# Performance work log

Hardware: AMD Instinct MI355X
Metric: run time of the kernel (lower is better)

## Reference

```python
import jax, jax.numpy as jnp
import numpy as np

B, N_E, E_DIM = 131072, 1024, 64
BETA = 0.25


def setup_inputs() -> dict:
    key = jax.random.key(0)
    kz, kw = jax.random.split(key)
    z = jax.random.normal(kz, (B, E_DIM), dtype=jnp.float32)
    # nn.Embedding init: uniform(-1/n_e, 1/n_e)
    emb_w = jax.random.uniform(kw, (N_E, E_DIM), dtype=jnp.float32,
                               minval=-1.0 / N_E, maxval=1.0 / N_E)
    return {"z": z, "emb_w": emb_w}


def reference(z, emb_w):
    beta = jnp.float32(BETA)
    # pairwise squared distances: [B, n_e]
    d = (jnp.sum(z * z, axis=1, keepdims=True)
         + jnp.sum(emb_w * emb_w, axis=1)
         - 2.0 * jnp.einsum('bd,nd->bn', z, emb_w))
    idx = jnp.argmin(d, axis=1)                      # [B]
    z_q = jnp.take(emb_w, idx, axis=0)               # [B, e_dim]
    # legacy=False branch
    loss = (beta * jnp.mean((jax.lax.stop_gradient(z_q) - z) ** 2)
            + jnp.mean((z_q - jax.lax.stop_gradient(z)) ** 2))
    # straight-through estimator
    z_q_st = z + jax.lax.stop_gradient(z_q - z)
    # torch.var is unbiased (ddof=1)
    v = jnp.var(idx.astype(jnp.float32), ddof=1)
    return (z_q_st, loss, idx, v)
```

## Files before the change

### kernel.cpp

```cpp
#include <hip/hip_runtime.h>
#include <stdint.h>


typedef __attribute__((ext_vector_type(8))) __bf16 bf16x8;
typedef __attribute__((ext_vector_type(4))) float f32x4;

#define OUT_LOSS 8388608
#define OUT_IDX  8388609
#define OUT_VAR  8519681

#define WS_LOSS  0
#define WS_S1    4096
#define WS_S2    8192
#define WS_EFRAG 12288
#define WS_EE    143360

__device__ __forceinline__ void gld_lds16(const void* g, void* l) {
  __builtin_amdgcn_global_load_lds(
      (const __attribute__((address_space(1))) unsigned*)g,
      (__attribute__((address_space(3))) unsigned*)l, 16, 0, 0);
}

__global__ void vq_prep(const float* __restrict__ emb, char* __restrict__ ws) {
  bf16x8* efrag = (bf16x8*)(ws + WS_EFRAG);
  float* eeoff = (float*)(ws + WS_EE);
  const int t = blockIdx.x;
  const int l = threadIdx.x;
  const int n = t * 16 + (l & 15);
  const int kb0 = (l >> 4) * 8;
  const float* er = emb + n * 64;
  for (int j = 0; j < 2; ++j) {
    const int kb = j * 32 + kb0;
    bf16x8 h;
#pragma unroll
    for (int i = 0; i < 8; ++i) h[i] = (__bf16)(-2.0f * er[kb + i]);
    efrag[(t * 2 + j) * 64 + l] = h;
  }
  if (l < 16) {
    const float* e2 = emb + (t * 16 + l) * 64;
    float s = 0.f;
#pragma unroll
    for (int d = 0; d < 64; ++d) s += e2[d] * e2[d];
    eeoff[t * 16 + l] = s + 0.5f;
  }
}

__global__ void __launch_bounds__(256) vq_main(
    const float* __restrict__ z, const float* __restrict__ emb,
    float* __restrict__ out, char* __restrict__ ws) {
  __shared__ char smfrag[2][16384];
  __shared__ float see[1024];
  __shared__ float sL[4];
  __shared__ int sA[4], sB[4];

  const int tid = threadIdx.x;
  const int wave = tid >> 6, lane = tid & 63;
  const int lr = lane & 15, ksl = lane >> 4;
  const int k0 = ksl * 8;
  const int row_base = blockIdx.x * 128 + wave * 32;

#define STAGE(ph, buf)                                                         \
  {                                                                            \
    _Pragma("unroll")                                                          \
    for (int i_ = 0; i_ < 4; ++i_)                                             \
      gld_lds16(ws + WS_EFRAG + (ph) * 16384 + i_ * 4096 + wave * 1024 + lane * 16, \
                smfrag[buf] + i_ * 4096 + wave * 1024);                        \
  }

  gld_lds16(ws + WS_EE + wave * 1024 + lane * 16, (char*)see + wave * 1024);
  STAGE(0, 0);
  STAGE(1, 1);

  bf16x8 zfa0, zfa1, zfb0, zfb1;
  float zza, zzb;
  {
    const float* zra = z + (size_t)(row_base + lr) * 64;
    const float* zrb = z + (size_t)(row_base + 16 + lr) * 64;
    f32x4 a0 = *(const f32x4*)(zra + k0);
    f32x4 a1 = *(const f32x4*)(zra + k0 + 4);
    f32x4 a2 = *(const f32x4*)(zra + 32 + k0);
    f32x4 a3 = *(const f32x4*)(zra + 32 + k0 + 4);
    f32x4 b0 = *(const f32x4*)(zrb + k0);
    f32x4 b1 = *(const f32x4*)(zrb + k0 + 4);
    f32x4 b2 = *(const f32x4*)(zrb + 32 + k0);
    f32x4 b3 = *(const f32x4*)(zrb + 32 + k0 + 4);
    float sa = 0.f, sb = 0.f;
#pragma unroll
    for (int i = 0; i < 4; ++i) {
      zfa0[i] = (__bf16)a0[i]; zfa0[4 + i] = (__bf16)a1[i];
      zfa1[i] = (__bf16)a2[i]; zfa1[4 + i] = (__bf16)a3[i];
      zfb0[i] = (__bf16)b0[i]; zfb0[4 + i] = (__bf16)b1[i];
      zfb1[i] = (__bf16)b2[i]; zfb1[4 + i] = (__bf16)b3[i];
      sa += a0[i] * a0[i] + a1[i] * a1[i] + a2[i] * a2[i] + a3[i] * a3[i];
      sb += b0[i] * b0[i] + b1[i] * b1[i] + b2[i] * b2[i] + b3[i] * b3[i];
    }
    sa += __shfl_xor(sa, 16, 64); sa += __shfl_xor(sa, 32, 64);
    sb += __shfl_xor(sb, 16, 64); sb += __shfl_xor(sb, 32, 64);
    zza = sa; zzb = sb;
  }

  unsigned rka = 0xFFFFFFFFu, rkb = 0xFFFFFFFFu;
  const unsigned k4 = (unsigned)(ksl * 4);

#pragma unroll
  for (int ph = 0; ph < 8; ++ph) {
    if (ph < 7) { asm volatile("s_waitcnt vmcnt(4)" ::: "memory"); }
    else       { asm volatile("s_waitcnt vmcnt(0)" ::: "memory"); }
    __builtin_amdgcn_sched_barrier(0);
    __builtin_amdgcn_s_barrier();
    const bf16x8* sfrag = (const bf16x8*)(smfrag[ph & 1]);
#pragma unroll
    for (int tt = 0; tt < 8; ++tt) {
      const int g = ph * 8 + tt;
      bf16x8 e0 = sfrag[(tt * 2 + 0) * 64 + lane];
      bf16x8 e1 = sfrag[(tt * 2 + 1) * 64 + lane];
      const f32x4 ee = *(const f32x4*)(see + g * 16 + ksl * 4);
      f32x4 a = __builtin_amdgcn_mfma_f32_16x16x32_bf16(e0, zfa0, ee, 0, 0, 0);
      a = __builtin_amdgcn_mfma_f32_16x16x32_bf16(e1, zfa1, a, 0, 0, 0);
      f32x4 b = __builtin_amdgcn_mfma_f32_16x16x32_bf16(e0, zfb0, ee, 0, 0, 0);
      b = __builtin_amdgcn_mfma_f32_16x16x32_bf16(e1, zfb1, b, 0, 0, 0);
      const unsigned tw = (unsigned)(g * 16);
      {
        const unsigned t0 = (__float_as_uint(a[0]) & 0xFFFFFC00u) | (k4 + 0);
        const unsigned t1 = (__float_as_uint(a[1]) & 0xFFFFFC00u) | (k4 + 1);
        const unsigned t2 = (__float_as_uint(a[2]) & 0xFFFFFC00u) | (k4 + 2);
        const unsigned t3 = (__float_as_uint(a[3]) & 0xFFFFFC00u) | (k4 + 3);
        rka = min(rka, min(min(t0, t1), min(t2, t3)) | tw);
      }
      {
        const unsigned t0 = (__float_as_uint(b[0]) & 0xFFFFFC00u) | (k4 + 0);
        const unsigned t1 = (__float_as_uint(b[1]) & 0xFFFFFC00u) | (k4 + 1);
        const unsigned t2 = (__float_as_uint(b[2]) & 0xFFFFFC00u) | (k4 + 2);
        const unsigned t3 = (__float_as_uint(b[3]) & 0xFFFFFC00u) | (k4 + 3);
        rkb = min(rkb, min(min(t0, t1), min(t2, t3)) | tw);
      }
    }
    __builtin_amdgcn_s_barrier();
    if (ph < 6) STAGE(ph + 2, ph & 1);
  }
#undef STAGE

  rka = min(rka, (unsigned)__shfl_xor((int)rka, 16, 64));
  rka = min(rka, (unsigned)__shfl_xor((int)rka, 32, 64));
  rkb = min(rkb, (unsigned)__shfl_xor((int)rkb, 16, 64));
  rkb = min(rkb, (unsigned)__shfl_xor((int)rkb, 32, 64));

  const int erow = lane >> 1, eseg = lane & 1;
  const int src = erow & 15;
  const unsigned ka = (unsigned)__shfl((int)rka, src, 64);
  const unsigned kb = (unsigned)__shfl((int)rkb, src, 64);
  const float za = __shfl(zza, src, 64);
  const float zb = __shfl(zzb, src, 64);
  const unsigned k = (erow < 16) ? ka : kb;
  const float zzv = (erow < 16) ? za : zb;
  const unsigned idx = k & 1023u;
  const size_t rowg = (size_t)row_base + erow;
  const f32x4* ep = (const f32x4*)(emb + (size_t)idx * 64 + eseg * 32);
  f32x4* op = (f32x4*)(out + rowg * 64 + eseg * 32);
#pragma unroll
  for (int c = 0; c < 8; ++c) op[c] = ep[c];

  float ls = 0.f; int s1 = 0, s2 = 0;
  if (eseg == 0) {
    ls = zzv + __uint_as_float(k & 0xFFFFFC00u) - 0.5f;
    s1 = (int)idx;
    s2 = (int)(idx * idx);
    out[OUT_IDX + rowg] = (float)idx;
  }
#pragma unroll
  for (int off = 1; off < 64; off <<= 1) {
    ls += __shfl_xor(ls, off, 64);
    s1 += __shfl_xor(s1, off, 64);
    s2 += __shfl_xor(s2, off, 64);
  }
  if (lane == 0) { sL[wave] = ls; sA[wave] = s1; sB[wave] = s2; }
  __syncthreads();
  if (tid == 0) {
    float L = 0; int a = 0, b = 0;
#pragma unroll
    for (int w = 0; w < 4; ++w) { L += sL[w]; a += sA[w]; b += sB[w]; }
    ((float*)(ws + WS_LOSS))[blockIdx.x] = L;
    ((int*)(ws + WS_S1))[blockIdx.x] = a;
    ((int*)(ws + WS_S2))[blockIdx.x] = b;
  }
}

__global__ void vq_final(float* __restrict__ out, const char* __restrict__ ws) {
  const int t = threadIdx.x;
  const float* lp = (const float*)(ws + WS_LOSS);
  const int* p1 = (const int*)(ws + WS_S1);
  const int* p2 = (const int*)(ws + WS_S2);
  double L = 0; long long a = 0, b = 0;
#pragma unroll
  for (int kk = 0; kk < 4; ++kk) {
    const int i = t + 256 * kk;
    L += (double)lp[i];
    a += (long long)p1[i];
    b += (long long)p2[i];
  }
#pragma unroll
  for (int off = 1; off < 64; off <<= 1) {
    L += __shfl_xor(L, off, 64);
    a += __shfl_xor(a, off, 64);
    b += __shfl_xor(b, off, 64);
  }
  __shared__ double sL[4];
  __shared__ long long sA[4], sB[4];
  const int wave = t >> 6, lane = t & 63;
  if (lane == 0) { sL[wave] = L; sA[wave] = a; sB[wave] = b; }
  __syncthreads();
  if (t == 0) {
    double Lt = 0; long long at = 0, bt = 0;
#pragma unroll
    for (int w = 0; w < 4; ++w) { Lt += sL[w]; at += sA[w]; bt += sB[w]; }
    out[OUT_LOSS] = (float)(1.25 * Lt / 8388608.0);
    long long num = bt * 131072LL - at * at;
    out[OUT_VAR] = (float)((double)num / (131072.0 * 131071.0));
  }
}

extern "C" void kernel_launch(void* const* d_in, const int* in_sizes, int n_in,
                              void* d_out, int out_size, void* d_ws, size_t ws_size,
                              hipStream_t stream) {
  (void)in_sizes; (void)n_in; (void)out_size; (void)ws_size;
  const float* z = (const float*)d_in[0];
  const float* emb = (const float*)d_in[1];
  float* out = (float*)d_out;
  char* ws = (char*)d_ws;
  vq_prep<<<64, 64, 0, stream>>>(emb, ws);
  vq_main<<<1024, 256, 0, stream>>>(z, emb, out, ws);
  vq_final<<<1, 256, 0, stream>>>(out, ws);
}
```

Measured before the change: 45.70 us.

## Use 512-thread blocks with triple-buffered LDS codebook staging and denser argmin keys

Blocks grow to 8 waves handling 256 rows each, so every codebook fragment staged into LDS is reused by twice as many rows. The LDS ring goes from two buffers to three, which lets the next prefetch be issued right after the barrier and removes the second barrier per phase. MFMA sections get raised wave priority, and the z loads are issued before the staging loads. The argmin key changes from masking the low mantissa bits to shifting the float left by 10, with a 0.875 bias so distances stay within a fixed exponent range, which keeps more mantissa precision in the key. The risk is lower occupancy and a distance-range assumption tied to the bias.

```diff
diff --git a/kernel.cpp b/kernel.cpp
--- a/kernel.cpp
+++ b/kernel.cpp
@@ -41,49 +41,51 @@
     float s = 0.f;
 #pragma unroll
     for (int d = 0; d < 64; ++d) s += e2[d] * e2[d];
-    eeoff[t * 16 + l] = s + 0.5f;
-  }
-}
-
-__global__ void __launch_bounds__(256) vq_main(
+    eeoff[t * 16 + l] = s + 0.875f;
+  }
+}
+
+__global__ void __launch_bounds__(512) vq_main(
     const float* __restrict__ z, const float* __restrict__ emb,
     float* __restrict__ out, char* __restrict__ ws) {
-  __shared__ char smfrag[2][16384];
+  __shared__ char smfrag[3][16384];
   __shared__ float see[1024];
-  __shared__ float sL[4];
-  __shared__ int sA[4], sB[4];
+  __shared__ float sL[8];
+  __shared__ int sA[8], sB[8];
 
   const int tid = threadIdx.x;
   const int wave = tid >> 6, lane = tid & 63;
   const int lr = lane & 15, ksl = lane >> 4;
   const int k0 = ksl * 8;
-  const int row_base = blockIdx.x * 128 + wave * 32;
-
-#define STAGE(ph, buf)                                                         \
-  {                                                                            \
-    _Pragma("unroll")                                                          \
-    for (int i_ = 0; i_ < 4; ++i_)                                             \
-      gld_lds16(ws + WS_EFRAG + (ph) * 16384 + i_ * 4096 + wave * 1024 + lane * 16, \
-                smfrag[buf] + i_ * 4096 + wave * 1024);                        \
-  }
-
-  gld_lds16(ws + WS_EE + wave * 1024 + lane * 16, (char*)see + wave * 1024);
+  const int row_base = blockIdx.x * 256 + wave * 32;
+
+#define STAGE(ph, buf)                                                          \
+  {                                                                             \
+    _Pragma("unroll")                                                           \
+    for (int i_ = 0; i_ < 2; ++i_)                                              \
+      gld_lds16(ws + WS_EFRAG + (ph) * 16384 + wave * 2048 + i_ * 1024 + lane * 16, \
+                smfrag[buf] + wave * 2048 + i_ * 1024);                         \
+  }
+
+  const float* zra = z + (size_t)(row_base + lr) * 64;
+  const float* zrb = z + (size_t)(row_base + 16 + lr) * 64;
+  f32x4 a0 = *(const f32x4*)(zra + k0);
+  f32x4 a1 = *(const f32x4*)(zra + k0 + 4);
+  f32x4 a2 = *(const f32x4*)(zra + 32 + k0);
+  f32x4 a3 = *(const f32x4*)(zra + 32 + k0 + 4);
+  f32x4 b0 = *(const f32x4*)(zrb + k0);
+  f32x4 b1 = *(const f32x4*)(zrb + k0 + 4);
+  f32x4 b2 = *(const f32x4*)(zrb + 32 + k0);
+  f32x4 b3 = *(const f32x4*)(zrb + 32 + k0 + 4);
+
+  if (wave < 4)
+    gld_lds16(ws + WS_EE + wave * 1024 + lane * 16, (char*)see + wave * 1024);
   STAGE(0, 0);
   STAGE(1, 1);
 
   bf16x8 zfa0, zfa1, zfb0, zfb1;
   float zza, zzb;
   {
-    const float* zra = z + (size_t)(row_base + lr) * 64;
-    const float* zrb = z + (size_t)(row_base + 16 + lr) * 64;
-    f32x4 a0 = *(const f32x4*)(zra + k0);
-    f32x4 a1 = *(const f32x4*)(zra + k0 + 4);
-    f32x4 a2 = *(const f32x4*)(zra + 32 + k0);
-    f32x4 a3 = *(const f32x4*)(zra + 32 + k0 + 4);
-    f32x4 b0 = *(const f32x4*)(zrb + k0);
-    f32x4 b1 = *(const f32x4*)(zrb + k0 + 4);
-    f32x4 b2 = *(const f32x4*)(zrb + 32 + k0);
-    f32x4 b3 = *(const f32x4*)(zrb + 32 + k0 + 4);
     float sa = 0.f, sb = 0.f;
 #pragma unroll
     for (int i = 0; i < 4; ++i) {
@@ -100,15 +102,16 @@
   }
 
   unsigned rka = 0xFFFFFFFFu, rkb = 0xFFFFFFFFu;
-  const unsigned k4 = (unsigned)(ksl * 4);
-
-#pragma unroll
+  const unsigned kj0 = (unsigned)(ksl * 4), kj1 = kj0 + 1, kj2 = kj0 + 2, kj3 = kj0 + 3;
+
   for (int ph = 0; ph < 8; ++ph) {
-    if (ph < 7) { asm volatile("s_waitcnt vmcnt(4)" ::: "memory"); }
-    else       { asm volatile("s_waitcnt vmcnt(0)" ::: "memory"); }
+    if (ph < 7) { asm volatile("s_waitcnt vmcnt(2)" ::: "memory"); }
+    else        { asm volatile("s_waitcnt vmcnt(0)" ::: "memory"); }
     __builtin_amdgcn_sched_barrier(0);
     __builtin_amdgcn_s_barrier();
-    const bf16x8* sfrag = (const bf16x8*)(smfrag[ph & 1]);
+    if (ph < 6) STAGE(ph + 2, (ph + 2) % 3);
+    const bf16x8* sfrag = (const bf16x8*)(smfrag[ph % 3]);
+    __builtin_amdgcn_s_setprio(1);
 #pragma unroll
     for (int tt = 0; tt < 8; ++tt) {
       const int g = ph * 8 + tt;
@@ -119,24 +122,23 @@
       a = __builtin_amdgcn_mfma_f32_16x16x32_bf16(e1, zfa1, a, 0, 0, 0);
       f32x4 b = __builtin_amdgcn_mfma_f32_16x16x32_bf16(e0, zfb0, ee, 0, 0, 0);
       b = __builtin_amdgcn_mfma_f32_16x16x32_bf16(e1, zfb1, b, 0, 0, 0);
-      const unsigned tw = (unsigned)(g * 16);
+      const unsigned g16 = (unsigned)(g * 16);
       {
-        const unsigned t0 = (__float_as_uint(a[0]) & 0xFFFFFC00u) | (k4 + 0);
-        const unsigned t1 = (__float_as_uint(a[1]) & 0xFFFFFC00u) | (k4 + 1);
-        const unsigned t2 = (__float_as_uint(a[2]) & 0xFFFFFC00u) | (k4 + 2);
-        const unsigned t3 = (__float_as_uint(a[3]) & 0xFFFFFC00u) | (k4 + 3);
-        rka = min(rka, min(min(t0, t1), min(t2, t3)) | tw);
+        const unsigned q0 = (__float_as_uint(a[0]) << 10) + kj0;
+        const unsigned q1 = (__float_as_uint(a[1]) << 10) + kj1;
+        const unsigned q2 = (__float_as_uint(a[2]) << 10) + kj2;
+        const unsigned q3 = (__float_as_uint(a[3]) << 10) + kj3;
+        rka = min(rka, min(min(q0, q1), min(q2, q3)) + g16);
       }
       {
-        const unsigned t0 = (__float_as_uint(b[0]) & 0xFFFFFC00u) | (k4 + 0);
-        const unsigned t1 = (__float_as_uint(b[1]) & 0xFFFFFC00u) | (k4 + 1);
-        const unsigned t2 = (__float_as_uint(b[2]) & 0xFFFFFC00u) | (k4 + 2);
-        const unsigned t3 = (__float_as_uint(b[3]) & 0xFFFFFC00u) | (k4 + 3);
-        rkb = min(rkb, min(min(t0, t1), min(t2, t3)) | tw);
+        const unsigned q0 = (__float_as_uint(b[0]) << 10) + kj0;
+        const unsigned q1 = (__float_as_uint(b[1]) << 10) + kj1;
+        const unsigned q2 = (__float_as_uint(b[2]) << 10) + kj2;
+        const unsigned q3 = (__float_as_uint(b[3]) << 10) + kj3;
+        rkb = min(rkb, min(min(q0, q1), min(q2, q3)) + g16);
       }
     }
-    __builtin_amdgcn_s_barrier();
-    if (ph < 6) STAGE(ph + 2, ph & 1);
+    __builtin_amdgcn_s_setprio(0);
   }
 #undef STAGE
 
@@ -162,7 +164,7 @@
 
   float ls = 0.f; int s1 = 0, s2 = 0;
   if (eseg == 0) {
-    ls = zzv + __uint_as_float(k & 0xFFFFFC00u) - 0.5f;
+    ls = zzv + __uint_as_float(0x3F400000u | (k >> 10)) - 0.875f;
     s1 = (int)idx;
     s2 = (int)(idx * idx);
     out[OUT_IDX + rowg] = (float)idx;
@@ -178,7 +180,7 @@
   if (tid == 0) {
     float L = 0; int a = 0, b = 0;
 #pragma unroll
-    for (int w = 0; w < 4; ++w) { L += sL[w]; a += sA[w]; b += sB[w]; }
+    for (int w = 0; w < 8; ++w) { L += sL[w]; a += sA[w]; b += sB[w]; }
     ((float*)(ws + WS_LOSS))[blockIdx.x] = L;
     ((int*)(ws + WS_S1))[blockIdx.x] = a;
     ((int*)(ws + WS_S2))[blockIdx.x] = b;
@@ -192,7 +194,7 @@
   const int* p2 = (const int*)(ws + WS_S2);
   double L = 0; long long a = 0, b = 0;
 #pragma unroll
-  for (int kk = 0; kk < 4; ++kk) {
+  for (int kk = 0; kk < 2; ++kk) {
     const int i = t + 256 * kk;
     L += (double)lp[i];
     a += (long long)p1[i];
@@ -204,15 +206,15 @@
     a += __shfl_xor(a, off, 64);
     b += __shfl_xor(b, off, 64);
   }
-  __shared__ double sL[4];
-  __shared__ long long sA[4], sB[4];
+  __shared__ double sLf[4];
+  __shared__ long long sAf[4], sBf[4];
   const int wave = t >> 6, lane = t & 63;
-  if (lane == 0) { sL[wave] = L; sA[wave] = a; sB[wave] = b; }
+  if (lane == 0) { sLf[wave] = L; sAf[wave] = a; sBf[wave] = b; }
   __syncthreads();
   if (t == 0) {
     double Lt = 0; long long at = 0, bt = 0;
 #pragma unroll
-    for (int w = 0; w < 4; ++w) { Lt += sL[w]; at += sA[w]; bt += sB[w]; }
+    for (int w = 0; w < 4; ++w) { Lt += sLf[w]; at += sAf[w]; bt += sBf[w]; }
     out[OUT_LOSS] = (float)(1.25 * Lt / 8388608.0);
     long long num = bt * 131072LL - at * at;
     out[OUT_VAR] = (float)((double)num / (131072.0 * 131071.0));
@@ -228,6 +230,6 @@
   float* out = (float*)d_out;
   char* ws = (char*)d_ws;
   vq_prep<<<64, 64, 0, stream>>>(emb, ws);
-  vq_main<<<1024, 256, 0, stream>>>(z, emb, out, ws);
+  vq_main<<<512, 512, 0, stream>>>(z, emb, out, ws);
   vq_final<<<1, 256, 0, stream>>>(out, ws);
 }
```

Result: no change. 45.92 us (+0.5%).
